# Kernel tuning notes

Measured on AMD Instinct MI355X. Metric: run time of the kernel, lower is better.

Reference implementation:

```python
import jax, jax.numpy as jnp
from jax import lax
import numpy as np

FEAT_STRIDE = 16
RATIOS = np.array([0.5, 1.0, 2.0])
SCALES = np.array([8.0, 16.0, 32.0])
PRE_NMS = 6000
POST_NMS = 300
NMS_THRESH = 0.7
MIN_SIZE = 16.0
A = 9  # num anchors per location


def _whctrs(a):
    w = a[2] - a[0] + 1.0
    h = a[3] - a[1] + 1.0
    return w, h, a[0] + 0.5 * (w - 1.0), a[1] + 0.5 * (h - 1.0)


def _mkanchors(ws, hs, cx, cy):
    return np.stack([cx - 0.5 * (ws - 1.0), cy - 0.5 * (hs - 1.0),
                     cx + 0.5 * (ws - 1.0), cy + 0.5 * (hs - 1.0)], axis=1)


def generate_anchors(base_size=16):
    base = np.array([1.0, 1.0, base_size, base_size]) - 1.0
    w, h, cx, cy = _whctrs(base)
    size = w * h
    ws = np.round(np.sqrt(size / RATIOS))
    hs = np.round(ws * RATIOS)
    ratio_anchors = _mkanchors(ws, hs, cx, cy)
    out = []
    for ra in ratio_anchors:
        w, h, cx, cy = _whctrs(ra)
        out.append(_mkanchors(w * SCALES, h * SCALES, cx, cy))
    return np.concatenate(out, axis=0).astype(np.float32)  # [9,4]


def setup_inputs() -> dict:
    key = jax.random.key(0)
    k1, k2 = jax.random.split(key)
    scores = jax.random.normal(k1, (1, 2 * A, 50, 80), dtype=jnp.float32)
    bbox_deltas = jax.random.normal(k2, (1, 4 * A, 50, 80), dtype=jnp.float32) * 0.5
    im_info = jnp.array([[800.0, 1280.0, 1.5]], dtype=jnp.float32)  # (h, w, scale)
    return {"scores": scores, "bbox_deltas": bbox_deltas, "im_info": im_info}


def reference(scores, bbox_deltas, im_info):
    base_anchors = jnp.asarray(generate_anchors())  # [A,4]
    H, W = scores.shape[-2], scores.shape[-1]

    # fg scores, flattened in (h, w, a) order to match anchor ordering
    sc = scores[:, A:, :, :].transpose(0, 2, 3, 1).reshape(-1)  # [K*A]

    # anchors for every feature-map location
    sx = (jnp.arange(W) * FEAT_STRIDE).astype(jnp.float32)
    sy = (jnp.arange(H) * FEAT_STRIDE).astype(jnp.float32)
    gy, gx = jnp.meshgrid(sy, sx, indexing="ij")
    shifts = jnp.stack([gx, gy, gx, gy], axis=-1).reshape(-1, 1, 4)  # [K,1,4]
    anchors = (base_anchors[None, :, :] + shifts).reshape(-1, 4)    # [K*A,4]

    # decode deltas (dw/dh clamped to [-10,10])
    d = bbox_deltas.transpose(0, 2, 3, 1).reshape(-1, 4)
    d = jnp.concatenate([d[:, :2], jnp.clip(d[:, 2:], -10.0, 10.0)], axis=1)
    aw = anchors[:, 2] - anchors[:, 0] + 1.0
    ah = anchors[:, 3] - anchors[:, 1] + 1.0
    acx = anchors[:, 0] + 0.5 * aw
    acy = anchors[:, 1] + 0.5 * ah
    pcx = d[:, 0] * aw + acx
    pcy = d[:, 1] * ah + acy
    pw = jnp.exp(d[:, 2]) * aw
    ph = jnp.exp(d[:, 3]) * ah
    boxes = jnp.stack([pcx - 0.5 * pw, pcy - 0.5 * ph,
                       pcx + 0.5 * pw, pcy + 0.5 * ph], axis=1)

    # clip to image
    im_h, im_w, im_s = im_info[0, 0], im_info[0, 1], im_info[0, 2]
    boxes = jnp.stack([
        jnp.clip(boxes[:, 0], 0.0, im_w - 1.0),
        jnp.clip(boxes[:, 1], 0.0, im_h - 1.0),
        jnp.clip(boxes[:, 2], 0.0, im_w - 1.0),
        jnp.clip(boxes[:, 3], 0.0, im_h - 1.0),
    ], axis=1)

    # min-size filter (masking instead of compaction, for static shapes)
    ws = boxes[:, 2] - boxes[:, 0] + 1.0
    hs = boxes[:, 3] - boxes[:, 1] + 1.0
    min_sz = MIN_SIZE * im_s
    valid = (ws >= min_sz) & (hs >= min_sz)
    sc = jnp.where(valid, sc, -jnp.inf)

    # pre-NMS top-k by score
    top_sc, top_idx = lax.top_k(sc, PRE_NMS)
    props = boxes[top_idx]  # [P,4], sorted by descending score
    alive0 = jnp.isfinite(top_sc)

    # pairwise IoU (the +1 pixel convention matching the rest of the pipeline)
    x1, y1, x2, y2 = props[:, 0], props[:, 1], props[:, 2], props[:, 3]
    areas = (x2 - x1 + 1.0) * (y2 - y1 + 1.0)
    iw = jnp.clip(jnp.minimum(x2[:, None], x2[None, :]) - jnp.maximum(x1[:, None], x1[None, :]) + 1.0, 0.0)
    ih = jnp.clip(jnp.minimum(y2[:, None], y2[None, :]) - jnp.maximum(y1[:, None], y1[None, :]) + 1.0, 0.0)
    inter = iw * ih
    iou = inter / (areas[:, None] + areas[None, :] - inter)  # [P,P] ~144MB

    idx = jnp.arange(PRE_NMS)

    def body(i, keep):
        sup = keep[i] & (iou[i] > NMS_THRESH) & (idx > i)
        return keep & ~sup

    keep = lax.fori_loop(0, PRE_NMS, body, alive0)

    # gather first POST_NMS kept proposals into fixed-size output [POST_NMS,5]
    rank = jnp.cumsum(keep) - 1
    dest = jnp.where(keep & (rank < POST_NMS), rank, POST_NMS)
    out = jnp.zeros((POST_NMS + 1, 5), dtype=scores.dtype)
    out = out.at[dest, 1:].set(props)
    return out[:POST_NMS]
```

## Files before the change

kernel.cpp:

```cpp
#include <hip/hip_runtime.h>
#include <stdint.h>

#define A_NUM 9
#define H_FM 50
#define W_FM 80
#define HW (H_FM * W_FM)
#define N_ANCH (A_NUM * HW)
#define PRE_NMS_N 6000
#define POST_NMS_N 300
#define NMS_TH 0.7f
#define MASK_W 94
#define MASK_STRIDE 96
#define NBIN 4096
#define BIN_CAP 4096
#define NBD 141
#define MASK_TILES (24 * 94)

typedef unsigned long long ull;

__constant__ float c_aw[9] = {184.f,368.f,736.f,128.f,256.f,512.f, 88.f,176.f,352.f};
__constant__ float c_ah[9] = { 96.f,192.f,384.f,128.f,256.f,512.f,176.f,352.f,704.f};

__device__ int    g_hist[NBIN];
__device__ ull    g_dead[MASK_STRIDE];
__device__ ull    g_rowany[MASK_STRIDE];
__device__ float4 g_boxes[N_ANCH];
__device__ float4 g_props[PRE_NMS_N];
__device__ ull    g_mask[(size_t)PRE_NMS_N * MASK_STRIDE];
__device__ ull    g_colsup[MASK_W * 64];

__global__ __launch_bounds__(256) void k_decode(const float* __restrict__ scores,
                                                const float* __restrict__ deltas,
                                                const float* __restrict__ iminfo,
                                                ull* __restrict__ bins) {
    int t = blockIdx.x * 256 + threadIdx.x;
    if (t >= N_ANCH) return;
    int a    = t / HW;
    int cell = t - a * HW;
    int x    = cell % W_FM;
    int y    = cell / W_FM;

    float sc = scores[(A_NUM + a) * HW + cell];

    int dbase = (a * 4) * HW + cell;
    float d0 = deltas[dbase];
    float d1 = deltas[dbase + HW];
    float d2 = deltas[dbase + 2 * HW];
    float d3 = deltas[dbase + 3 * HW];
    d2 = fminf(fmaxf(d2, -10.f), 10.f);
    d3 = fminf(fmaxf(d3, -10.f), 10.f);

    float aw = c_aw[a], ah = c_ah[a];
    float acx = (float)(x * 16 + 8);
    float acy = (float)(y * 16 + 8);

    float pcx = d0 * aw + acx;
    float pcy = d1 * ah + acy;
    float pw  = expf(d2) * aw;
    float ph  = expf(d3) * ah;

    float x1 = pcx - 0.5f * pw;
    float y1 = pcy - 0.5f * ph;
    float x2 = pcx + 0.5f * pw;
    float y2 = pcy + 0.5f * ph;

    float imh = iminfo[0], imw = iminfo[1], ims = iminfo[2];
    x1 = fminf(fmaxf(x1, 0.f), imw - 1.f);
    y1 = fminf(fmaxf(y1, 0.f), imh - 1.f);
    x2 = fminf(fmaxf(x2, 0.f), imw - 1.f);
    y2 = fminf(fmaxf(y2, 0.f), imh - 1.f);

    float wsz = x2 - x1 + 1.f;
    float hsz = y2 - y1 + 1.f;
    float minsz = 16.f * ims;
    bool valid = (wsz >= minsz) && (hsz >= minsz);

    g_boxes[t] = make_float4(x1, y1, x2, y2);

    unsigned int u   = __float_as_uint(sc);
    unsigned int asc = (u & 0x80000000u) ? ~u : (u | 0x80000000u);
    unsigned int dk  = ~asc;
    if (!valid) dk = 0xFF800000u;

    unsigned int ikey = (unsigned int)(cell * A_NUM + a);
    ull key = ((ull)dk << 32) | ikey;

    int bin  = (int)(dk >> 20);
    int slot = atomicAdd(&g_hist[bin], 1);
    if (slot < BIN_CAP) bins[(size_t)bin * BIN_CAP + slot] = key;
}

__global__ __launch_bounds__(256) void k_binsort(const ull* __restrict__ bins) {
    __shared__ ull sb[4096];
    __shared__ int red[256];
    int b = blockIdx.x;
    int cntf = g_hist[b];
    if (cntf == 0) return;
    int tid = threadIdx.x;

    int part = 0;
    for (int j = tid; j < b; j += 256) part += g_hist[j];
    red[tid] = part;
    __syncthreads();
    for (int off = 128; off > 0; off >>= 1) {
        if (tid < off) red[tid] += red[tid + off];
        __syncthreads();
    }
    int s0 = red[0];
    if (s0 >= PRE_NMS_N) return;

    int cnt = (cntf < BIN_CAP) ? cntf : BIN_CAP;
    const ull* seg = bins + (size_t)b * BIN_CAP;

    int P = 2; while (P < cnt) P <<= 1;
    for (int i = tid; i < P; i += 256) sb[i] = (i < cnt) ? seg[i] : ~0ULL;
    __syncthreads();
    for (int k2 = 2; k2 <= P; k2 <<= 1) {
        for (int j = k2 >> 1; j >= 1; j >>= 1) {
            for (int p = tid; p < (P >> 1); p += 256) {
                int i  = ((p & ~(j - 1)) << 1) | (p & (j - 1));
                int pr = i | j;
                bool up = ((i & k2) == 0);
                ull a = sb[i], c = sb[pr];
                if ((a > c) == up) { sb[i] = c; sb[pr] = a; }
            }
            __syncthreads();
        }
    }
    for (int i = tid; i < cnt; i += 256) {
        int r = s0 + i;
        if (r < PRE_NMS_N) {
            ull key = sb[i];
            unsigned int dk = (unsigned int)(key >> 32);
            if (dk < 0xFF800000u) {
                unsigned int ik = (unsigned int)key;
                int tt = (int)(ik % A_NUM) * HW + (int)(ik / A_NUM);
                g_props[r] = g_boxes[tt];
            } else {
                g_props[r] = make_float4(0.f, 0.f, 0.f, 0.f);
                atomicOr(&g_dead[r >> 6], 1ULL << (r & 63));
            }
        }
    }
}

__global__ __launch_bounds__(256) void k_maskcol() {
    __shared__ float4 sj[256];
    int vb = blockIdx.x;
    int tid = threadIdx.x;

    if (vb < 16) g_hist[vb * 256 + tid] = 0;

    if (vb < MASK_TILES) {
        int bx = vb % 24;
        int by = vb / 24;

        int li = tid & 63;
        int wl = tid >> 6;
        int i  = by * 64 + li;
        int w  = bx * 4 + wl;

        if (bx * 256 + 255 <= by * 64) {
            if (i < PRE_NMS_N && w < MASK_W)
                g_mask[(size_t)i * MASK_STRIDE + w] = 0ULL;
            return;
        }

        int jbase = bx * 256;
        int jj = jbase + tid;
        sj[tid] = (jj < PRE_NMS_N) ? g_props[jj] : make_float4(0.f, 0.f, 0.f, 0.f);
        __syncthreads();

        if (i >= PRE_NMS_N || w >= MASK_W) return;

        float4 bi = g_props[i];
        float ai = (bi.z - bi.x + 1.f) * (bi.w - bi.y + 1.f);
        ull bits = 0;
        int jstart = w * 64;
        int lbase = jstart - jbase;
        int bstart = i + 1 - jstart; if (bstart < 0) bstart = 0;
        int bend = PRE_NMS_N - jstart; if (bend > 64) bend = 64;
        for (int b = bstart; b < bend; ++b) {
            float4 bj = sj[lbase + b];
            float aj = (bj.z - bj.x + 1.f) * (bj.w - bj.y + 1.f);
            float iw = fminf(bi.z, bj.z) - fmaxf(bi.x, bj.x) + 1.f;
            float ih = fminf(bi.w, bj.w) - fmaxf(bi.y, bj.y) + 1.f;
            iw = fmaxf(iw, 0.f);
            ih = fmaxf(ih, 0.f);
            float inter = iw * ih;
            float iou = inter / (ai + aj - inter);
            if (iou > NMS_TH) bits |= (1ULL << b);
        }
        g_mask[(size_t)i * MASK_STRIDE + w] = bits;
        if (bits && w != (i >> 6)) atomicOr(&g_rowany[i >> 6], 1ULL << (i & 63));
    } else {
        int w = vb - MASK_TILES;
        int gj = w * 64 + tid;
        if (tid < 64)
            sj[tid] = (gj < PRE_NMS_N) ? g_props[gj] : make_float4(0.f, 0.f, 0.f, 0.f);
        __syncthreads();
        if (tid < 64) {
            float4 bj = sj[tid];
            float aj = (bj.z - bj.x + 1.f) * (bj.w - bj.y + 1.f);
            ull bits = 0;
            for (int b = 0; b < tid; ++b) {
                float4 bi = sj[b];
                float ai = (bi.z - bi.x + 1.f) * (bi.w - bi.y + 1.f);
                float iw = fminf(bi.z, bj.z) - fmaxf(bi.x, bj.x) + 1.f;
                float ih = fminf(bi.w, bj.w) - fmaxf(bi.y, bj.y) + 1.f;
                iw = fmaxf(iw, 0.f);
                ih = fmaxf(ih, 0.f);
                float inter = iw * ih;
                float iou = inter / (ai + aj - inter);
                if (iou > NMS_TH) bits |= (1ULL << b);
            }
            g_colsup[gj] = bits;
        }
    }
}

#define BATCH 8
__global__ __launch_bounds__(256, 1) void k_scan(float* __restrict__ out) {
    __shared__ ull scol[MASK_W * 64];
    __shared__ ull srow[MASK_W];
    __shared__ int s_kept[POST_NMS_N];
    __shared__ int s_kc;
    int tid = threadIdx.x;

    for (int i = tid; i < MASK_W * 64; i += 256) scol[i] = g_colsup[i];
    for (int i = tid; i < MASK_W; i += 256)      srow[i] = g_rowany[i];
    __syncthreads();

    if (tid < 64) {
        int lane = tid;
        ull rm0 = g_dead[lane];
        ull rm1 = (lane < MASK_W - 64) ? g_dead[64 + lane] : ~0ULL;
        if (lane == 29) rm1 |= 0xFFFF000000000000ULL;
        int kc = 0;
        int pw = -2;
        ull dnext = 0;

        for (;;) {
            ull avail0 = __ballot(~rm0 != 0ULL);
            ull avail1 = __ballot(~rm1 != 0ULL);
            int w;
            if (avail0)      w = __ffsll(avail0) - 1;
            else if (avail1) w = 63 + __ffsll(avail1);
            else break;

            ull diag = (w == pw + 1) ? dnext : scol[(w << 6) + lane];
            if (w + 1 < MASK_W) dnext = scol[((w + 1) << 6) + lane];
            pw = w;

            ull raw = srow[w];
            ull rmw = (w < 64) ? rm0 : rm1;
            int ri  = (w < 64) ? w : w - 64;
            unsigned clo = __builtin_amdgcn_readlane((unsigned)rmw, ri);
            unsigned chi = __builtin_amdgcn_readlane((unsigned)(rmw >> 32), ri);
            ull curw = ((ull)chi << 32) | clo;

            ull U = ~curw;
            ull K = 0;
            while (U) {
                ull UK = U | K;
                bool deadp = (diag & K)  != 0ULL;
                bool freep = (diag & UK) == 0ULL;
                ull nd = __ballot(deadp) & U;
                U &= ~nd;
                ull nk = __ballot(freep) & U;
                U &= ~nk;
                K |= nk;
                if (!nk && !nd) break;
            }

            int cnt  = __popcll(K);
            int take = min(cnt, POST_NMS_N - kc);
            if (K & (1ULL << lane)) {
                int pos = kc + __popcll(K & ((1ULL << lane) - 1ULL));
                if (pos < POST_NMS_N) s_kept[pos] = (w << 6) + lane;
            }
            kc += take;
            if (kc >= POST_NMS_N) break;

            if (w < 64) { if (lane == w)      rm0 = ~0ULL; }
            else        { if (lane == w - 64) rm1 = ~0ULL; }

            ull need = K & raw;
            while (need) {
                int id[BATCH];
                int n = 0;
#pragma unroll
                for (int t2 = 0; t2 < BATCH; ++t2) {
                    id[t2] = 0;
                    if (need) { id[t2] = __ffsll(need) - 1; need &= need - 1; n = t2 + 1; }
                }
                ull v0[BATCH], v1[BATCH];
#pragma unroll
                for (int t2 = 0; t2 < BATCH; ++t2) {
                    const ull* __restrict__ row =
                        g_mask + (size_t)((w << 6) + id[t2]) * MASK_STRIDE;
                    v0[t2] = row[lane];
                    v1[t2] = (lane < MASK_W - 64) ? row[64 + lane] : 0ULL;
                }
                ull a0 = 0, a1 = 0;
#pragma unroll
                for (int t2 = 0; t2 < BATCH; ++t2) {
                    ull m = (t2 < n) ? ~0ULL : 0ULL;
                    a0 |= v0[t2] & m;
                    a1 |= v1[t2] & m;
                }
                rm0 |= a0;
                rm1 |= a1;
            }
        }
        if (lane == 0) s_kc = (kc < POST_NMS_N) ? kc : POST_NMS_N;
    }
    __syncthreads();

    for (int i = tid; i < MASK_STRIDE; i += 256) {
        g_dead[i] = 0ULL;
        g_rowany[i] = 0ULL;
    }

    int kcf = s_kc;
    for (int r = tid; r < POST_NMS_N; r += 256) {
        float4 p = make_float4(0.f, 0.f, 0.f, 0.f);
        if (r < kcf) p = g_props[s_kept[r]];
        out[r * 5 + 0] = 0.f;
        out[r * 5 + 1] = p.x;
        out[r * 5 + 2] = p.y;
        out[r * 5 + 3] = p.z;
        out[r * 5 + 4] = p.w;
    }
}

extern "C" void kernel_launch(void* const* d_in, const int* in_sizes, int n_in,
                              void* d_out, int out_size, void* d_ws, size_t ws_size,
                              hipStream_t stream) {
    const float* scores = (const float*)d_in[0];
    const float* deltas = (const float*)d_in[1];
    const float* iminfo = (const float*)d_in[2];
    float* out = (float*)d_out;
    ull* bins = (ull*)d_ws;

    k_decode<<<NBD, 256, 0, stream>>>(scores, deltas, iminfo, bins);
    k_binsort<<<NBIN, 256, 0, stream>>>(bins);
    k_maskcol<<<MASK_TILES + MASK_W, 256, 0, stream>>>();
    k_scan<<<1, 256, 0, stream>>>(out);
}
```

Measured before the change: 113.8 us.

## Process NMS mask words in pairs with precomputed cross-block suppression

The serial NMS scan now resolves two adjacent 64-box words per iteration. A new cross-word suppression table (box pairs between an even word and the following odd word) is computed in the mask kernel and staged in shared memory, so the second word's in-word resolution can start without a round trip through global mask rows. Row-any flags now exclude the paired neighbour word, and mask-row fetches are batched across both words. This roughly halves the number of serial iterations and ballot/readlane steps, at the cost of extra IoU work and shared memory.

```diff
diff --git a/kernel.cpp b/kernel.cpp
--- a/kernel.cpp
+++ b/kernel.cpp
@@ -10,6 +10,7 @@
 #define POST_NMS_N 300
 #define NMS_TH 0.7f
 #define MASK_W 94
+#define NPAIR 47
 #define MASK_STRIDE 96
 #define NBIN 4096
 #define BIN_CAP 4096
@@ -28,6 +29,16 @@
 __device__ float4 g_props[PRE_NMS_N];
 __device__ ull    g_mask[(size_t)PRE_NMS_N * MASK_STRIDE];
 __device__ ull    g_colsup[MASK_W * 64];
+__device__ ull    g_csup[NPAIR * 64];
+
+__device__ __forceinline__ float iou_gt(float4 bi, float ai, float4 bj, float aj) {
+    float iw = fminf(bi.z, bj.z) - fmaxf(bi.x, bj.x) + 1.f;
+    float ih = fminf(bi.w, bj.w) - fmaxf(bi.y, bj.y) + 1.f;
+    iw = fmaxf(iw, 0.f);
+    ih = fmaxf(ih, 0.f);
+    float inter = iw * ih;
+    return inter / (ai + aj - inter);
+}
 
 __global__ __launch_bounds__(256) void k_decode(const float* __restrict__ scores,
                                                 const float* __restrict__ deltas,
@@ -183,21 +194,21 @@
         for (int b = bstart; b < bend; ++b) {
             float4 bj = sj[lbase + b];
             float aj = (bj.z - bj.x + 1.f) * (bj.w - bj.y + 1.f);
-            float iw = fminf(bi.z, bj.z) - fmaxf(bi.x, bj.x) + 1.f;
-            float ih = fminf(bi.w, bj.w) - fmaxf(bi.y, bj.y) + 1.f;
-            iw = fmaxf(iw, 0.f);
-            ih = fmaxf(ih, 0.f);
-            float inter = iw * ih;
-            float iou = inter / (ai + aj - inter);
-            if (iou > NMS_TH) bits |= (1ULL << b);
+            if (iou_gt(bi, ai, bj, aj) > NMS_TH) bits |= (1ULL << b);
         }
         g_mask[(size_t)i * MASK_STRIDE + w] = bits;
-        if (bits && w != (i >> 6)) atomicOr(&g_rowany[i >> 6], 1ULL << (i & 63));
+        int wi = i >> 6;
+        bool instep = (w == wi) || (((wi & 1) == 0) && (w == wi + 1));
+        if (bits && !instep) atomicOr(&g_rowany[wi], 1ULL << (i & 63));
     } else {
         int w = vb - MASK_TILES;
         int gj = w * 64 + tid;
         if (tid < 64)
             sj[tid] = (gj < PRE_NMS_N) ? g_props[gj] : make_float4(0.f, 0.f, 0.f, 0.f);
+        if ((w & 1) && tid >= 64 && tid < 128) {
+            int gj2 = (w - 1) * 64 + (tid - 64);
+            sj[tid] = (gj2 < PRE_NMS_N) ? g_props[gj2] : make_float4(0.f, 0.f, 0.f, 0.f);
+        }
         __syncthreads();
         if (tid < 64) {
             float4 bj = sj[tid];
@@ -206,15 +217,18 @@
             for (int b = 0; b < tid; ++b) {
                 float4 bi = sj[b];
                 float ai = (bi.z - bi.x + 1.f) * (bi.w - bi.y + 1.f);
-                float iw = fminf(bi.z, bj.z) - fmaxf(bi.x, bj.x) + 1.f;
-                float ih = fminf(bi.w, bj.w) - fmaxf(bi.y, bj.y) + 1.f;
-                iw = fmaxf(iw, 0.f);
-                ih = fmaxf(ih, 0.f);
-                float inter = iw * ih;
-                float iou = inter / (ai + aj - inter);
-                if (iou > NMS_TH) bits |= (1ULL << b);
+                if (iou_gt(bi, ai, bj, aj) > NMS_TH) bits |= (1ULL << b);
             }
             g_colsup[gj] = bits;
+            if (w & 1) {
+                ull cb = 0;
+                for (int b = 0; b < 64; ++b) {
+                    float4 bi = sj[64 + b];
+                    float ai = (bi.z - bi.x + 1.f) * (bi.w - bi.y + 1.f);
+                    if (iou_gt(bi, ai, bj, aj) > NMS_TH) cb |= (1ULL << b);
+                }
+                g_csup[(w >> 1) * 64 + tid] = cb;
+            }
         }
     }
 }
@@ -222,12 +236,14 @@
 #define BATCH 8
 __global__ __launch_bounds__(256, 1) void k_scan(float* __restrict__ out) {
     __shared__ ull scol[MASK_W * 64];
+    __shared__ ull scsup[NPAIR * 64];
     __shared__ ull srow[MASK_W];
     __shared__ int s_kept[POST_NMS_N];
     __shared__ int s_kc;
     int tid = threadIdx.x;
 
     for (int i = tid; i < MASK_W * 64; i += 256) scol[i] = g_colsup[i];
+    for (int i = tid; i < NPAIR * 64; i += 256)  scsup[i] = g_csup[i];
     for (int i = tid; i < MASK_W; i += 256)      srow[i] = g_rowany[i];
     __syncthreads();
 
@@ -237,8 +253,8 @@
         ull rm1 = (lane < MASK_W - 64) ? g_dead[64 + lane] : ~0ULL;
         if (lane == 29) rm1 |= 0xFFFF000000000000ULL;
         int kc = 0;
-        int pw = -2;
-        ull dnext = 0;
+        int ps = -2;
+        ull pA = 0, pB = 0, pC = 0;
 
         for (;;) {
             ull avail0 = __ballot(~rm0 != 0ULL);
@@ -248,57 +264,107 @@
             else if (avail1) w = 63 + __ffsll(avail1);
             else break;
 
-            ull diag = (w == pw + 1) ? dnext : scol[(w << 6) + lane];
-            if (w + 1 < MASK_W) dnext = scol[((w + 1) << 6) + lane];
-            pw = w;
-
-            ull raw = srow[w];
-            ull rmw = (w < 64) ? rm0 : rm1;
-            int ri  = (w < 64) ? w : w - 64;
-            unsigned clo = __builtin_amdgcn_readlane((unsigned)rmw, ri);
-            unsigned chi = __builtin_amdgcn_readlane((unsigned)(rmw >> 32), ri);
-            ull curw = ((ull)chi << 32) | clo;
-
-            ull U = ~curw;
-            ull K = 0;
+            int s  = w >> 1;
+            int w0 = s << 1;
+            int w1 = w0 | 1;
+
+            ull diagA, diagB, csup;
+            if (s == ps + 1) { diagA = pA; diagB = pB; csup = pC; }
+            else {
+                diagA = scol[(w0 << 6) + lane];
+                diagB = scol[(w1 << 6) + lane];
+                csup  = scsup[(s << 6) + lane];
+            }
+            if (s + 1 < NPAIR) {
+                pA = scol[((w0 + 2) << 6) + lane];
+                pB = scol[((w1 + 2) << 6) + lane];
+                pC = scsup[((s + 1) << 6) + lane];
+            }
+            ps = s;
+
+            ull raw0 = srow[w0], raw1 = srow[w1];
+
+            ull rmw0 = (w0 < 64) ? rm0 : rm1;
+            int ri0  = (w0 < 64) ? w0 : w0 - 64;
+            ull curw0 = ((ull)__builtin_amdgcn_readlane((unsigned)(rmw0 >> 32), ri0) << 32)
+                        | __builtin_amdgcn_readlane((unsigned)rmw0, ri0);
+            ull rmw1 = (w1 < 64) ? rm0 : rm1;
+            int ri1  = (w1 < 64) ? w1 : w1 - 64;
+            ull curw1 = ((ull)__builtin_amdgcn_readlane((unsigned)(rmw1 >> 32), ri1) << 32)
+                        | __builtin_amdgcn_readlane((unsigned)rmw1, ri1);
+
+            ull U = ~curw0, K0 = 0;
             while (U) {
-                ull UK = U | K;
-                bool deadp = (diag & K)  != 0ULL;
-                bool freep = (diag & UK) == 0ULL;
+                ull UK = U | K0;
+                bool deadp = (diagA & K0) != 0ULL;
+                bool freep = (diagA & UK) == 0ULL;
                 ull nd = __ballot(deadp) & U;
                 U &= ~nd;
                 ull nk = __ballot(freep) & U;
                 U &= ~nk;
-                K |= nk;
+                K0 |= nk;
                 if (!nk && !nd) break;
             }
 
-            int cnt  = __popcll(K);
-            int take = min(cnt, POST_NMS_N - kc);
-            if (K & (1ULL << lane)) {
-                int pos = kc + __popcll(K & ((1ULL << lane) - 1ULL));
-                if (pos < POST_NMS_N) s_kept[pos] = (w << 6) + lane;
-            }
-            kc += take;
+            ull U1 = ~curw1;
+            U1 &= ~__ballot((csup & K0) != 0ULL);
+            ull K1 = 0;
+            while (U1) {
+                ull UK = U1 | K1;
+                bool deadp = (diagB & K1) != 0ULL;
+                bool freep = (diagB & UK) == 0ULL;
+                ull nd = __ballot(deadp) & U1;
+                U1 &= ~nd;
+                ull nk = __ballot(freep) & U1;
+                U1 &= ~nk;
+                K1 |= nk;
+                if (!nk && !nd) break;
+            }
+
+            int cnt0 = __popcll(K0);
+            int take0 = min(cnt0, POST_NMS_N - kc);
+            if (K0 & (1ULL << lane)) {
+                int pos = kc + __popcll(K0 & ((1ULL << lane) - 1ULL));
+                if (pos < POST_NMS_N) s_kept[pos] = (w0 << 6) + lane;
+            }
+            kc += take0;
             if (kc >= POST_NMS_N) break;
 
-            if (w < 64) { if (lane == w)      rm0 = ~0ULL; }
-            else        { if (lane == w - 64) rm1 = ~0ULL; }
-
-            ull need = K & raw;
-            while (need) {
+            int cnt1 = __popcll(K1);
+            int take1 = min(cnt1, POST_NMS_N - kc);
+            if (K1 & (1ULL << lane)) {
+                int pos = kc + __popcll(K1 & ((1ULL << lane) - 1ULL));
+                if (pos < POST_NMS_N) s_kept[pos] = (w1 << 6) + lane;
+            }
+            kc += take1;
+            if (kc >= POST_NMS_N) break;
+
+            if (w0 < 64) { if (lane == w0)      rm0 = ~0ULL; }
+            else         { if (lane == w0 - 64) rm1 = ~0ULL; }
+            if (w1 < 64) { if (lane == w1)      rm0 = ~0ULL; }
+            else         { if (lane == w1 - 64) rm1 = ~0ULL; }
+
+            ull needA = K0 & raw0;
+            ull needB = K1 & raw1;
+            while (needA | needB) {
                 int id[BATCH];
                 int n = 0;
 #pragma unroll
                 for (int t2 = 0; t2 < BATCH; ++t2) {
                     id[t2] = 0;
-                    if (need) { id[t2] = __ffsll(need) - 1; need &= need - 1; n = t2 + 1; }
+                    if (needA) {
+                        int b = __ffsll(needA) - 1; needA &= needA - 1;
+                        id[t2] = (w0 << 6) + b; n = t2 + 1;
+                    } else if (needB) {
+                        int b = __ffsll(needB) - 1; needB &= needB - 1;
+                        id[t2] = (w1 << 6) + b; n = t2 + 1;
+                    }
                 }
                 ull v0[BATCH], v1[BATCH];
 #pragma unroll
                 for (int t2 = 0; t2 < BATCH; ++t2) {
                     const ull* __restrict__ row =
-                        g_mask + (size_t)((w << 6) + id[t2]) * MASK_STRIDE;
+                        g_mask + (size_t)id[t2] * MASK_STRIDE;
                     v0[t2] = row[lane];
                     v1[t2] = (lane < MASK_W - 64) ? row[64 + lane] : 0ULL;
                 }
```

Result: slower. 122.3 us (+7.5%).
